# Kernel tuning notes

Hardware: AMD Instinct MI355X
Metric: run time of the kernel (lower is better)

## Reference

```python
import jax, jax.numpy as jnp
import numpy as np

B, D, N = 32768, 128, 8
TEMP = 0.25          # episodic_memory_temperature
DECAY = 0.99         # episodic_strength_decay
AGE_INC = 0.02       # episodic_age_increment


def _l2norm(x, eps=1e-6):
    n = jnp.sqrt(jnp.sum(x * x, axis=-1, keepdims=True))
    return x / jnp.maximum(n, eps)


def setup_inputs() -> dict:
    key = jax.random.key(0)
    ks = jax.random.split(key, 16)
    s = 0.05
    inp = {
        'signal': jax.random.normal(ks[0], (B, D), jnp.float32),
        'previous': jax.random.normal(ks[1], (B, D), jnp.float32),
        'hidden': jax.random.normal(ks[2], (B, D), jnp.float32),
        'episodic_keys': jax.random.normal(ks[3], (B, N, D), jnp.float32),
        'episodic_values': jax.random.normal(ks[4], (B, N, D), jnp.float32),
        'episodic_strength': jax.random.uniform(ks[5], (B, N), jnp.float32),
        'episodic_age': jax.random.uniform(ks[6], (B, N), jnp.float32),
        # Linear weights stored as [in, out] (torch stores [out, in]); small random
        # instead of the zero init so gradients flow for kernel testing.
        'w_read_query': jax.random.normal(ks[7], (2 * D, D), jnp.float32) * s,
        'w_read_mix': jax.random.normal(ks[8], (2 * D, 1), jnp.float32) * s,
        'b_read_mix': jnp.full((1,), -0.2, jnp.float32),
        'w_key': jax.random.normal(ks[9], (2 * D, D), jnp.float32) * s,
        'b_key': jnp.zeros((D,), jnp.float32),
        'w_value': jax.random.normal(ks[10], (2 * D, D), jnp.float32) * s,
        'b_value': jnp.zeros((D,), jnp.float32),
        'w_write': jax.random.normal(ks[11], (2 * D, 1), jnp.float32) * s,
        'b_write': jnp.full((1,), -0.6, jnp.float32),
        'w_persist': jax.random.normal(ks[12], (2 * D, 1), jnp.float32) * s,
        'b_persist': jnp.zeros((1,), jnp.float32),
        'w_merge': jax.random.normal(ks[13], (2 * D, 1), jnp.float32) * s,
        'b_merge': jnp.zeros((1,), jnp.float32),
    }
    return inp


def reference(signal, previous, hidden, episodic_keys, episodic_values,
              episodic_strength, episodic_age,
              w_read_query, w_read_mix, b_read_mix, w_key, b_key, w_value,
              b_value, w_write, b_write, w_persist, b_persist, w_merge, b_merge):
    dtype = signal.dtype
    n_slots = episodic_keys.shape[1]

    # ---------------- read ----------------
    sp = jnp.concatenate([signal, previous], axis=-1)             # [B, 2D]
    query = _l2norm(sp @ w_read_query)                            # [B, D]
    norm_keys = _l2norm(episodic_keys)                            # [B, N, D]
    content_scores = jnp.einsum('bd,bnd->bn', query, norm_keys)   # [B, N]
    content_w = jax.nn.softmax(content_scores / TEMP, axis=-1)
    content_read = jnp.einsum('bn,bnd->bd', content_w, episodic_values)
    persistent_scores = 2.4 * episodic_strength + 0.6 * (1.0 - episodic_age)
    persistent_w = jax.nn.softmax(persistent_scores / TEMP, axis=-1)
    persistent_read = jnp.einsum('bn,bnd->bd', persistent_w, episodic_values)
    read_mix = jax.nn.sigmoid(sp @ w_read_mix + b_read_mix)       # [B, 1]
    memory_read = read_mix * content_read + (1.0 - read_mix) * persistent_read

    # ---------------- write ----------------
    joined = jnp.concatenate([signal, hidden], axis=-1)           # [B, 2D]
    candidate_key = jnp.tanh(joined @ w_key + b_key)              # [B, D]
    candidate_value = jnp.tanh(joined @ w_value + b_value)        # [B, D]
    write_strength = jax.nn.sigmoid(joined @ w_write + b_write)   # [B, 1]
    persistence = jax.nn.sigmoid(joined @ w_persist + b_persist)  # [B, 1]
    similarity = jnp.einsum('bd,bnd->bn', _l2norm(candidate_key), norm_keys)

    top_k = min(3, n_slots)
    top_sim, top_idx = jax.lax.top_k(similarity, top_k)           # [B, 3]
    max_sim = top_sim[:, 0]
    merge_index = top_idx[:, 0]
    second_sim = top_sim[:, 1]
    novelty = jnp.clip(1.0 - max_sim, 0.0, 1.0)[:, None]          # [B, 1]

    replace_scores = (1.2 * episodic_age + 1.0 * (1.0 - episodic_strength)
                      + 0.5 * (1.0 - similarity))
    replace_index = jnp.argmax(replace_scores, axis=-1)
    merge_pref = jax.nn.sigmoid(joined @ w_merge + b_merge + 2.6 * max_sim[:, None])

    full_m = (max_sim > 0.78) & (merge_pref[:, 0] >= 0.55)
    multi_m = full_m & (second_sim > 0.68)
    partial_m = (~multi_m) & (max_sim > 0.64) & (second_sim > 0.52)

    rows = jnp.arange(signal.shape[0])[:, None]
    target_w = jax.nn.one_hot(replace_index, n_slots, dtype=dtype)
    partial_w = jax.nn.softmax(top_sim[:, :2] / TEMP, axis=-1)
    partial_target = jnp.zeros_like(target_w).at[rows, top_idx[:, :2]].add(partial_w)
    multi_w = jax.nn.softmax(top_sim / TEMP, axis=-1)
    multi_target = jnp.zeros_like(target_w).at[rows, top_idx].add(multi_w)
    full_target = jax.nn.one_hot(merge_index, n_slots, dtype=dtype)

    target_w = jnp.where(full_m[:, None], full_target, target_w)
    target_w = jnp.where(partial_m[:, None], partial_target, target_w)
    target_w = jnp.where(multi_m[:, None], multi_target, target_w)

    scale = jnp.where(multi_m[:, None], 0.16 + 0.52 * write_strength,
                      jnp.where(partial_m[:, None], 0.18 + 0.62 * write_strength,
                                0.20 + 0.80 * write_strength))
    overwrite = target_w * scale * (0.55 + 0.45 * novelty)        # [B, N]
    ow3 = overwrite[..., None]                                    # [B, N, 1]

    merge_like = full_m | partial_m | multi_m
    key_mix = jnp.where(merge_like[:, None], 0.28 + 0.24 * persistence,
                        0.78 + 0.16 * persistence)[:, :, None]    # [B, 1, 1]
    value_mix = jnp.where(merge_like[:, None], 0.42 + 0.28 * persistence,
                          0.82 + 0.12 * persistence)[:, :, None]

    updated_keys = episodic_keys + ow3 * key_mix * (candidate_key[:, None, :] - episodic_keys)
    updated_values = episodic_values + ow3 * value_mix * (candidate_value[:, None, :] - episodic_values)

    boost = overwrite * (0.45 + 0.35 * persistence + 0.45 * novelty + 0.25 * write_strength)
    updated_strength = jnp.clip(episodic_strength * DECAY + boost, 0.0, 1.0)
    updated_age = jnp.clip((episodic_age + AGE_INC) * (1.0 - overwrite), 0.0, 1.0)

    return memory_read, updated_keys, updated_values, updated_strength, updated_age
```

## Files before the change

### kernel.cpp

```cpp
#include <hip/hip_runtime.h>
#include <cstddef>

#define BD 128
#define NS 8
#define ROWS 32
#define BLOCK 256

typedef float __attribute__((ext_vector_type(2))) f32x2;

__device__ __forceinline__ float sigm(float x) { return 1.0f / (1.0f + __expf(-x)); }

__device__ __forceinline__ void nt_store2(float2 v, float2* p) {
    f32x2 t; t.x = v.x; t.y = v.y;
    __builtin_nontemporal_store(t, (f32x2*)p);
}

__global__ __launch_bounds__(BLOCK, 3)
void sbcore_kernel(
    const float* __restrict__ g_signal, const float* __restrict__ g_prev,
    const float* __restrict__ g_hidden, const float* __restrict__ g_keys,
    const float* __restrict__ g_vals, const float* __restrict__ g_str,
    const float* __restrict__ g_age,
    const float* __restrict__ w_rq, const float* __restrict__ w_mix,
    const float* __restrict__ b_mix, const float* __restrict__ w_key,
    const float* __restrict__ b_key, const float* __restrict__ w_val,
    const float* __restrict__ b_val, const float* __restrict__ w_wr,
    const float* __restrict__ b_wr, const float* __restrict__ w_pe,
    const float* __restrict__ b_pe, const float* __restrict__ w_mg,
    const float* __restrict__ b_mg,
    float* __restrict__ o_read, float* __restrict__ o_keys,
    float* __restrict__ o_vals, float* __restrict__ o_str,
    float* __restrict__ o_age)
{
    __shared__ __align__(16) float sig_s[ROWS][BD];
    __shared__ __align__(16) float prv_s[ROWS][BD];
    __shared__ __align__(16) float hid_s[ROWS][BD];
    __shared__ __align__(16) float str_s[ROWS*NS], age_s[ROWS*NS];
    __shared__ float red_s[4][16][2];
    __shared__ float ckinv_s[ROWS];
    __shared__ __align__(16) float head_s[ROWS][4];

    const int tid = threadIdx.x;
    const int row0 = blockIdx.x * ROWS;

    {
        const float4* gs4 = (const float4*)(g_signal + (size_t)row0 * BD);
        const float4* gp4 = (const float4*)(g_prev   + (size_t)row0 * BD);
        const float4* gh4 = (const float4*)(g_hidden + (size_t)row0 * BD);
#pragma unroll
        for (int it = 0; it < (ROWS*BD/4)/BLOCK; ++it) {
            int i = tid + it*BLOCK;
            int r = i >> 5, d4 = i & 31;
            *(float4*)&sig_s[r][d4*4] = gs4[i];
            *(float4*)&prv_s[r][d4*4] = gp4[i];
            *(float4*)&hid_s[r][d4*4] = gh4[i];
        }
    }
    str_s[tid] = g_str[(size_t)row0*NS + tid];
    age_s[tid] = g_age[(size_t)row0*NS + tid];
    __syncthreads();

    {
        const int hr = tid >> 3;
        const int hh = (tid >> 1) & 3;
        const int hj = tid & 1;
        const float* ws = (hh==0) ? w_mix : (hh==1) ? w_wr : (hh==2) ? w_pe : w_mg;
        const float4* w4p = (const float4*)(ws + hj*BD);
        const float*  xr  = (hj==0) ? &sig_s[hr][0]
                                    : ((hh==0) ? &prv_s[hr][0] : &hid_s[hr][0]);
        const float4* x4p = (const float4*)xr;
        float p = 0.f;
#pragma unroll
        for (int q = 0; q < 32; ++q) {
            const float4 w4 = w4p[q];
            const float4 x4 = x4p[q];
            p = fmaf(x4.w, w4.w, fmaf(x4.z, w4.z, fmaf(x4.y, w4.y, fmaf(x4.x, w4.x, p))));
        }
        p += __shfl_xor(p, 1);
        if (hj == 0) head_s[hr][hh] = p;
    }

    const int d    = tid & (BD-1);
    const int h    = tid >> 7;
    const int wave = tid >> 6;
    const int lane = tid & 63;

    float aq[16], ak[16], av[16];
#pragma unroll
    for (int r = 0; r < 16; ++r) { aq[r] = 0.f; ak[r] = 0.f; av[r] = 0.f; }

    for (int kk = 0; kk < BD; kk += 4) {
        float wq0 = w_rq[(kk+0)*BD + d], wq1 = w_rq[(kk+1)*BD + d],
              wq2 = w_rq[(kk+2)*BD + d], wq3 = w_rq[(kk+3)*BD + d];
        float wk0 = w_key[(kk+0)*BD + d], wk1 = w_key[(kk+1)*BD + d],
              wk2 = w_key[(kk+2)*BD + d], wk3 = w_key[(kk+3)*BD + d];
        float wv0 = w_val[(kk+0)*BD + d], wv1 = w_val[(kk+1)*BD + d],
              wv2 = w_val[(kk+2)*BD + d], wv3 = w_val[(kk+3)*BD + d];
#pragma unroll
        for (int r = 0; r < 16; ++r) {
            const float4 s4 = *(const float4*)&sig_s[h*16 + r][kk];
            aq[r] = fmaf(s4.w, wq3, fmaf(s4.z, wq2, fmaf(s4.y, wq1, fmaf(s4.x, wq0, aq[r]))));
            ak[r] = fmaf(s4.w, wk3, fmaf(s4.z, wk2, fmaf(s4.y, wk1, fmaf(s4.x, wk0, ak[r]))));
            av[r] = fmaf(s4.w, wv3, fmaf(s4.z, wv2, fmaf(s4.y, wv1, fmaf(s4.x, wv0, av[r]))));
        }
    }
    for (int kk = 0; kk < BD; kk += 4) {
        const int k = kk + BD;
        float wq0 = w_rq[(k+0)*BD + d], wq1 = w_rq[(k+1)*BD + d],
              wq2 = w_rq[(k+2)*BD + d], wq3 = w_rq[(k+3)*BD + d];
        float wk0 = w_key[(k+0)*BD + d], wk1 = w_key[(k+1)*BD + d],
              wk2 = w_key[(k+2)*BD + d], wk3 = w_key[(k+3)*BD + d];
        float wv0 = w_val[(k+0)*BD + d], wv1 = w_val[(k+1)*BD + d],
              wv2 = w_val[(k+2)*BD + d], wv3 = w_val[(k+3)*BD + d];
#pragma unroll
        for (int r = 0; r < 16; ++r) {
            const float4 p4 = *(const float4*)&prv_s[h*16 + r][kk];
            const float4 h4 = *(const float4*)&hid_s[h*16 + r][kk];
            aq[r] = fmaf(p4.w, wq3, fmaf(p4.z, wq2, fmaf(p4.y, wq1, fmaf(p4.x, wq0, aq[r]))));
            ak[r] = fmaf(h4.w, wk3, fmaf(h4.z, wk2, fmaf(h4.y, wk1, fmaf(h4.x, wk0, ak[r]))));
            av[r] = fmaf(h4.w, wv3, fmaf(h4.z, wv2, fmaf(h4.y, wv1, fmaf(h4.x, wv0, av[r]))));
        }
    }

    const float bk = b_key[d], bv = b_val[d];
    float ckr[16], cvr[16], q2[16], c2[16];
#pragma unroll
    for (int r = 0; r < 16; ++r) {
        ckr[r] = tanhf(ak[r] + bk);
        cvr[r] = tanhf(av[r] + bv);
        q2[r]  = aq[r] * aq[r];
        c2[r]  = ckr[r] * ckr[r];
    }
#pragma unroll
    for (int off = 32; off > 0; off >>= 1) {
#pragma unroll
        for (int r = 0; r < 16; ++r) {
            q2[r] += __shfl_xor(q2[r], off);
            c2[r] += __shfl_xor(c2[r], off);
        }
    }
    if (lane == 0) {
#pragma unroll
        for (int r = 0; r < 16; ++r) { red_s[wave][r][0] = q2[r]; red_s[wave][r][1] = c2[r]; }
    }
    __syncthreads();
#pragma unroll
    for (int r = 0; r < 16; ++r) {
        float sq = red_s[h*2][r][0] + red_s[h*2+1][r][0];
        float sc = red_s[h*2][r][1] + red_s[h*2+1][r][1];
        float qi = 1.0f / fmaxf(sqrtf(sq), 1e-6f);
        sig_s[h*16 + r][d] = aq[r] * qi;
        prv_s[h*16 + r][d] = ckr[r];
        hid_s[h*16 + r][d] = cvr[r];
        if (d == 0) ckinv_s[h*16 + r] = 1.0f / fmaxf(sqrtf(sc), 1e-6f);
    }
    __syncthreads();

    const float bmix = b_mix[0], bwr = b_wr[0], bpe = b_pe[0], bmg = b_mg[0];
    const int sj = lane & 7;

    for (int rr = 0; rr < 8; ++rr) {
        const int r = wave*8 + rr;
        const size_t row = (size_t)row0 + r;
        const size_t kvb = row * (size_t)(NS*BD);

        const float4* kp4  = (const float4*)(g_keys + kvb);
        const float4* qrow = (const float4*)&sig_s[r][0];
        const float4* crow = (const float4*)&prv_s[r][0];
        float pk = 0.f, pq = 0.f, pc = 0.f;
#pragma unroll
        for (int q = 0; q < 4; ++q) {
            const float4 k4 = kp4[4*lane + q];
            const float4 q4 = qrow[sj*4 + q];
            const float4 c4 = crow[sj*4 + q];
            pk = fmaf(k4.w,k4.w, fmaf(k4.z,k4.z, fmaf(k4.y,k4.y, fmaf(k4.x,k4.x, pk))));
            pq = fmaf(q4.w,k4.w, fmaf(q4.z,k4.z, fmaf(q4.y,k4.y, fmaf(q4.x,k4.x, pq))));
            pc = fmaf(c4.w,k4.w, fmaf(c4.z,k4.z, fmaf(c4.y,k4.y, fmaf(c4.x,k4.x, pc))));
        }
        const float2* vp = (const float2*)(g_vals + kvb);
        float2 vf[NS];
#pragma unroll
        for (int n = 0; n < NS; ++n) vf[n] = vp[n*64 + lane];
        const float2 cki = *(const float2*)&prv_s[r][2*lane];
        const float2 cvi = *(const float2*)&hid_s[r][2*lane];

        pk += __shfl_xor(pk, 1); pk += __shfl_xor(pk, 2); pk += __shfl_xor(pk, 4);
        pq += __shfl_xor(pq, 1); pq += __shfl_xor(pq, 2); pq += __shfl_xor(pq, 4);
        pc += __shfl_xor(pc, 1); pc += __shfl_xor(pc, 2); pc += __shfl_xor(pc, 4);
        const float ki   = 1.0f / fmaxf(sqrtf(pk), 1e-6f);
        const float csn  = pq * ki;
        const float simn = pc * ki * ckinv_s[r];
        float cs[NS], sim[NS];
#pragma unroll
        for (int m = 0; m < NS; ++m) {
            cs[m]  = __shfl(csn,  m*8);
            sim[m] = __shfl(simn, m*8);
        }

        const float4 hd = *(const float4*)&head_s[r][0];
        const float mix   = sigm(hd.x + bmix);
        const float wsv   = sigm(hd.y + bwr);
        const float pev   = sigm(hd.z + bpe);
        const float mglin = hd.w + bmg;

        float mC = cs[0];
#pragma unroll
        for (int n = 1; n < NS; ++n) mC = fmaxf(mC, cs[n]);
        float eC[NS], sC = 0.f;
#pragma unroll
        for (int n = 0; n < NS; ++n) { eC[n] = __expf((cs[n]-mC)*4.0f); sC += eC[n]; }
        const float4 st0 = *(const float4*)&str_s[r*NS];
        const float4 st1 = *(const float4*)&str_s[r*NS+4];
        const float4 ag0 = *(const float4*)&age_s[r*NS];
        const float4 ag1 = *(const float4*)&age_s[r*NS+4];
        const float stv[NS] = {st0.x,st0.y,st0.z,st0.w,st1.x,st1.y,st1.z,st1.w};
        const float agv[NS] = {ag0.x,ag0.y,ag0.z,ag0.w,ag1.x,ag1.y,ag1.z,ag1.w};
        float psc[NS]; float mP = -1e30f;
#pragma unroll
        for (int n = 0; n < NS; ++n) {
            psc[n] = fmaf(2.4f, stv[n], 0.6f*(1.0f - agv[n]));
            mP = fmaxf(mP, psc[n]);
        }
        float eP[NS], sP = 0.f;
#pragma unroll
        for (int n = 0; n < NS; ++n) { eP[n] = __expf((psc[n]-mP)*4.0f); sP += eP[n]; }
        const float icS = 1.0f/sC, ipS = 1.0f/sP;

        float2 cr = make_float2(0.f, 0.f), prd = make_float2(0.f, 0.f);
#pragma unroll
        for (int n = 0; n < NS; ++n) {
            float wc = eC[n]*icS, wp = eP[n]*ipS;
            cr.x  = fmaf(wc, vf[n].x, cr.x);  cr.y  = fmaf(wc, vf[n].y, cr.y);
            prd.x = fmaf(wp, vf[n].x, prd.x); prd.y = fmaf(wp, vf[n].y, prd.y);
        }
        float2 mr;
        mr.x = mix*cr.x + (1.0f-mix)*prd.x;
        mr.y = mix*cr.y + (1.0f-mix)*prd.y;
        nt_store2(mr, &((float2*)(o_read + row*BD))[lane]);

        float tv0 = -1e30f; int ti0 = 0;
#pragma unroll
        for (int n = 0; n < NS; ++n) if (sim[n] > tv0) { tv0 = sim[n]; ti0 = n; }
        float tv1 = -1e30f; int ti1 = 0;
#pragma unroll
        for (int n = 0; n < NS; ++n) {
            float v = (n == ti0) ? -1e30f : sim[n];
            if (v > tv1) { tv1 = v; ti1 = n; }
        }
        float tv2 = -1e30f; int ti2 = 0;
#pragma unroll
        for (int n = 0; n < NS; ++n) {
            float v = (n == ti0 || n == ti1) ? -1e30f : sim[n];
            if (v > tv2) { tv2 = v; ti2 = n; }
        }

        float rm = -1e30f; int ri = 0;
#pragma unroll
        for (int n = 0; n < NS; ++n) {
            float rsv = fmaf(1.2f, agv[n], (1.0f - stv[n])) + 0.5f*(1.0f - sim[n]);
            if (rsv > rm) { rm = rsv; ri = n; }
        }

        const float mpref = sigm(mglin + 2.6f*tv0);
        const bool full  = (tv0 > 0.78f) && (mpref >= 0.55f);
        const bool multi = full && (tv1 > 0.68f);
        const bool part  = (!multi) && (tv0 > 0.64f) && (tv1 > 0.52f);
        const float nov  = fminf(fmaxf(1.0f - tv0, 0.0f), 1.0f);

        float a0, a1, a2, aR;
        if (multi) {
            float e1 = __expf((tv1 - tv0)*4.0f), e2 = __expf((tv2 - tv0)*4.0f);
            float inv = 1.0f/(1.0f + e1 + e2);
            a0 = inv; a1 = e1*inv; a2 = e2*inv; aR = 0.f;
        } else if (part) {
            float e1 = __expf((tv1 - tv0)*4.0f);
            float inv = 1.0f/(1.0f + e1);
            a0 = inv; a1 = e1*inv; a2 = 0.f; aR = 0.f;
        } else if (full) {
            a0 = 1.f; a1 = 0.f; a2 = 0.f; aR = 0.f;
        } else {
            a0 = 0.f; a1 = 0.f; a2 = 0.f; aR = 1.f;
        }

        const float scl = multi ? fmaf(0.52f, wsv, 0.16f)
                        : part  ? fmaf(0.62f, wsv, 0.18f)
                                : fmaf(0.80f, wsv, 0.20f);
        const bool  mlike = full || part || multi;
        const float km  = mlike ? fmaf(0.24f, pev, 0.28f) : fmaf(0.16f, pev, 0.78f);
        const float vm  = mlike ? fmaf(0.28f, pev, 0.42f) : fmaf(0.12f, pev, 0.82f);
        const float owc = scl * fmaf(0.45f, nov, 0.55f);
        const float bco = 0.45f + 0.35f*pev + 0.45f*nov + 0.25f*wsv;

        const float2* kp2 = (const float2*)(g_keys + kvb);
        float2* okp = (float2*)(o_keys + kvb);
        float2* ovp = (float2*)(o_vals + kvb);
#pragma unroll
        for (int n = 0; n < NS; ++n) {
            const float2 kf2 = kp2[n*64 + lane];
            float tn = ((n==ti0) ? a0 : (n==ti1) ? a1 : (n==ti2) ? a2 : 0.f)
                     + ((n==ri) ? aR : 0.f);
            float ow = tn*owc;
            float a = ow*km, b2 = ow*vm;
            float2 uk, uv;
            uk.x = fmaf(a,  cki.x - kf2.x, kf2.x);
            uk.y = fmaf(a,  cki.y - kf2.y, kf2.y);
            uv.x = fmaf(b2, cvi.x - vf[n].x, vf[n].x);
            uv.y = fmaf(b2, cvi.y - vf[n].y, vf[n].y);
            nt_store2(uk, &okp[n*64 + lane]);
            nt_store2(uv, &ovp[n*64 + lane]);
        }
        if (lane < NS) {
            float tn = ((lane==ti0) ? a0 : (lane==ti1) ? a1 : (lane==ti2) ? a2 : 0.f)
                     + ((lane==ri) ? aR : 0.f);
            float ow = tn*owc;
            float us = fminf(fmaxf(fmaf(str_s[r*NS+lane], 0.99f, ow*bco), 0.f), 1.f);
            float ua = fminf(fmaxf((age_s[r*NS+lane] + 0.02f)*(1.0f - ow), 0.f), 1.f);
            o_str[row*NS + lane] = us;
            o_age[row*NS + lane] = ua;
        }
    }
}

extern "C" void kernel_launch(void* const* d_in, const int* in_sizes, int n_in,
                              void* d_out, int out_size, void* d_ws, size_t ws_size,
                              hipStream_t stream) {
    const float* g_signal = (const float*)d_in[0];
    const float* g_prev   = (const float*)d_in[1];
    const float* g_hidden = (const float*)d_in[2];
    const float* g_keys   = (const float*)d_in[3];
    const float* g_vals   = (const float*)d_in[4];
    const float* g_str    = (const float*)d_in[5];
    const float* g_age    = (const float*)d_in[6];
    const float* w_rq     = (const float*)d_in[7];
    const float* w_mix    = (const float*)d_in[8];
    const float* b_mix    = (const float*)d_in[9];
    const float* w_key    = (const float*)d_in[10];
    const float* b_key    = (const float*)d_in[11];
    const float* w_val    = (const float*)d_in[12];
    const float* b_val    = (const float*)d_in[13];
    const float* w_wr     = (const float*)d_in[14];
    const float* b_wr     = (const float*)d_in[15];
    const float* w_pe     = (const float*)d_in[16];
    const float* b_pe     = (const float*)d_in[17];
    const float* w_mg     = (const float*)d_in[18];
    const float* b_mg     = (const float*)d_in[19];

    const size_t B = (size_t)in_sizes[0] / BD;
    float* out   = (float*)d_out;
    float* o_read = out;
    float* o_keys = o_read + B*BD;
    float* o_vals = o_keys + B*NS*BD;
    float* o_str  = o_vals + B*NS*BD;
    float* o_age  = o_str  + B*NS;

    const int blocks = (int)(B / ROWS);
    sbcore_kernel<<<dim3(blocks), dim3(BLOCK), 0, stream>>>(
        g_signal, g_prev, g_hidden, g_keys, g_vals, g_str, g_age,
        w_rq, w_mix, b_mix, w_key, b_key, w_val, b_val,
        w_wr, b_wr, w_pe, b_pe, w_mg, b_mg,
        o_read, o_keys, o_vals, o_str, o_age);
}
```

Measured before the change: 651.1 us.

## Shrink block to 4 rows and split projection K across waves

Cuts rows per block from 32 to 4, so the grid grows eightfold and each wave handles one memory row. The three projection matmuls are reorganised so each wave covers a K-slice with float4 weight columns, and partial sums are reduced through shared memory. The 4 per-row head dot products are now spread over 16 lanes each. This aims for more parallelism and latency hiding in the memory-bound phase, at the cost of rereading the three weight matrices far more often (eight times as many blocks) and adding an extra reduction step.

Measured after the change: 613.3 us. 1.06x faster.

```diff
diff --git a/kernel.cpp b/kernel.cpp
--- a/kernel.cpp
+++ b/kernel.cpp
@@ -3,9 +3,10 @@
 
 #define BD 128
 #define NS 8
-#define ROWS 32
+#define ROWS 4
 #define BLOCK 256
 
+typedef float __attribute__((ext_vector_type(4))) f32x4;
 typedef float __attribute__((ext_vector_type(2))) f32x2;
 
 __device__ __forceinline__ float sigm(float x) { return 1.0f / (1.0f + __expf(-x)); }
@@ -35,132 +36,153 @@
     __shared__ __align__(16) float sig_s[ROWS][BD];
     __shared__ __align__(16) float prv_s[ROWS][BD];
     __shared__ __align__(16) float hid_s[ROWS][BD];
-    __shared__ __align__(16) float str_s[ROWS*NS], age_s[ROWS*NS];
-    __shared__ float red_s[4][16][2];
-    __shared__ float ckinv_s[ROWS];
+    __shared__ __align__(16) f32x4 part_s[4][3][ROWS][32];
+    __shared__ float str_s[ROWS*NS], age_s[ROWS*NS];
     __shared__ __align__(16) float head_s[ROWS][4];
 
     const int tid = threadIdx.x;
     const int row0 = blockIdx.x * ROWS;
 
+    if (tid < ROWS*32) {
+        int r = tid >> 5, d4 = tid & 31;
+        size_t gb = (size_t)(row0 + r) * 32 + d4;
+        *(float4*)&sig_s[r][d4*4] = ((const float4*)g_signal)[gb];
+        *(float4*)&prv_s[r][d4*4] = ((const float4*)g_prev)[gb];
+        *(float4*)&hid_s[r][d4*4] = ((const float4*)g_hidden)[gb];
+    }
+    if (tid < ROWS*NS) {
+        str_s[tid] = g_str[(size_t)row0*NS + tid];
+        age_s[tid] = g_age[(size_t)row0*NS + tid];
+    }
+    __syncthreads();
+
     {
-        const float4* gs4 = (const float4*)(g_signal + (size_t)row0 * BD);
-        const float4* gp4 = (const float4*)(g_prev   + (size_t)row0 * BD);
-        const float4* gh4 = (const float4*)(g_hidden + (size_t)row0 * BD);
-#pragma unroll
-        for (int it = 0; it < (ROWS*BD/4)/BLOCK; ++it) {
-            int i = tid + it*BLOCK;
-            int r = i >> 5, d4 = i & 31;
-            *(float4*)&sig_s[r][d4*4] = gs4[i];
-            *(float4*)&prv_s[r][d4*4] = gp4[i];
-            *(float4*)&hid_s[r][d4*4] = gh4[i];
-        }
-    }
-    str_s[tid] = g_str[(size_t)row0*NS + tid];
-    age_s[tid] = g_age[(size_t)row0*NS + tid];
-    __syncthreads();
-
-    {
-        const int hr = tid >> 3;
-        const int hh = (tid >> 1) & 3;
-        const int hj = tid & 1;
+        const int dotid = tid >> 4;
+        const int hr = dotid >> 2;
+        const int hh = dotid & 3;
+        const int hj = tid & 15;
         const float* ws = (hh==0) ? w_mix : (hh==1) ? w_wr : (hh==2) ? w_pe : w_mg;
-        const float4* w4p = (const float4*)(ws + hj*BD);
-        const float*  xr  = (hj==0) ? &sig_s[hr][0]
-                                    : ((hh==0) ? &prv_s[hr][0] : &hid_s[hr][0]);
-        const float4* x4p = (const float4*)xr;
+        const float* xb = (hj < 8) ? &sig_s[hr][0]
+                        : (((hh==0) ? &prv_s[hr][0] : &hid_s[hr][0]) - BD);
         float p = 0.f;
 #pragma unroll
-        for (int q = 0; q < 32; ++q) {
-            const float4 w4 = w4p[q];
-            const float4 x4 = x4p[q];
+        for (int q = 0; q < 4; ++q) {
+            const int k = hj*16 + q*4;
+            const float4 w4 = *(const float4*)&ws[k];
+            const float4 x4 = *(const float4*)&xb[k];
             p = fmaf(x4.w, w4.w, fmaf(x4.z, w4.z, fmaf(x4.y, w4.y, fmaf(x4.x, w4.x, p))));
         }
-        p += __shfl_xor(p, 1);
+        p += __shfl_xor(p, 1); p += __shfl_xor(p, 2);
+        p += __shfl_xor(p, 4); p += __shfl_xor(p, 8);
         if (hj == 0) head_s[hr][hh] = p;
     }
 
-    const int d    = tid & (BD-1);
-    const int h    = tid >> 7;
     const int wave = tid >> 6;
     const int lane = tid & 63;
-
-    float aq[16], ak[16], av[16];
-#pragma unroll
-    for (int r = 0; r < 16; ++r) { aq[r] = 0.f; ak[r] = 0.f; av[r] = 0.f; }
-
-    for (int kk = 0; kk < BD; kk += 4) {
-        float wq0 = w_rq[(kk+0)*BD + d], wq1 = w_rq[(kk+1)*BD + d],
-              wq2 = w_rq[(kk+2)*BD + d], wq3 = w_rq[(kk+3)*BD + d];
-        float wk0 = w_key[(kk+0)*BD + d], wk1 = w_key[(kk+1)*BD + d],
-              wk2 = w_key[(kk+2)*BD + d], wk3 = w_key[(kk+3)*BD + d];
-        float wv0 = w_val[(kk+0)*BD + d], wv1 = w_val[(kk+1)*BD + d],
-              wv2 = w_val[(kk+2)*BD + d], wv3 = w_val[(kk+3)*BD + d];
-#pragma unroll
-        for (int r = 0; r < 16; ++r) {
-            const float4 s4 = *(const float4*)&sig_s[h*16 + r][kk];
-            aq[r] = fmaf(s4.w, wq3, fmaf(s4.z, wq2, fmaf(s4.y, wq1, fmaf(s4.x, wq0, aq[r]))));
-            ak[r] = fmaf(s4.w, wk3, fmaf(s4.z, wk2, fmaf(s4.y, wk1, fmaf(s4.x, wk0, ak[r]))));
-            av[r] = fmaf(s4.w, wv3, fmaf(s4.z, wv2, fmaf(s4.y, wv1, fmaf(s4.x, wv0, av[r]))));
-        }
-    }
-    for (int kk = 0; kk < BD; kk += 4) {
-        const int k = kk + BD;
-        float wq0 = w_rq[(k+0)*BD + d], wq1 = w_rq[(k+1)*BD + d],
-              wq2 = w_rq[(k+2)*BD + d], wq3 = w_rq[(k+3)*BD + d];
-        float wk0 = w_key[(k+0)*BD + d], wk1 = w_key[(k+1)*BD + d],
-              wk2 = w_key[(k+2)*BD + d], wk3 = w_key[(k+3)*BD + d];
-        float wv0 = w_val[(k+0)*BD + d], wv1 = w_val[(k+1)*BD + d],
-              wv2 = w_val[(k+2)*BD + d], wv3 = w_val[(k+3)*BD + d];
-#pragma unroll
-        for (int r = 0; r < 16; ++r) {
-            const float4 p4 = *(const float4*)&prv_s[h*16 + r][kk];
-            const float4 h4 = *(const float4*)&hid_s[h*16 + r][kk];
-            aq[r] = fmaf(p4.w, wq3, fmaf(p4.z, wq2, fmaf(p4.y, wq1, fmaf(p4.x, wq0, aq[r]))));
-            ak[r] = fmaf(h4.w, wk3, fmaf(h4.z, wk2, fmaf(h4.y, wk1, fmaf(h4.x, wk0, ak[r]))));
-            av[r] = fmaf(h4.w, wv3, fmaf(h4.z, wv2, fmaf(h4.y, wv1, fmaf(h4.x, wv0, av[r]))));
-        }
-    }
-
-    const float bk = b_key[d], bv = b_val[d];
-    float ckr[16], cvr[16], q2[16], c2[16];
-#pragma unroll
-    for (int r = 0; r < 16; ++r) {
-        ckr[r] = tanhf(ak[r] + bk);
-        cvr[r] = tanhf(av[r] + bv);
-        q2[r]  = aq[r] * aq[r];
-        c2[r]  = ckr[r] * ckr[r];
-    }
-#pragma unroll
-    for (int off = 32; off > 0; off >>= 1) {
-#pragma unroll
-        for (int r = 0; r < 16; ++r) {
-            q2[r] += __shfl_xor(q2[r], off);
-            c2[r] += __shfl_xor(c2[r], off);
-        }
-    }
-    if (lane == 0) {
-#pragma unroll
-        for (int r = 0; r < 16; ++r) { red_s[wave][r][0] = q2[r]; red_s[wave][r][1] = c2[r]; }
+    const int hi   = lane >> 5;
+    const int dg   = lane & 31;
+
+    {
+        const int kbase = hi ? (BD + wave*32) : (wave*32);
+        const f32x4* wq4 = (const f32x4*)w_rq;
+        const f32x4* wk4 = (const f32x4*)w_key;
+        const f32x4* wv4 = (const f32x4*)w_val;
+        const int wi0 = kbase*32 + dg;
+        const float* x1b = hi ? &prv_s[0][0] : &sig_s[0][0];
+        const float* x2b = hi ? &hid_s[0][0] : &sig_s[0][0];
+        const int xo = wave*32;
+
+        f32x4 aq[ROWS], ak[ROWS], av[ROWS];
+#pragma unroll
+        for (int r = 0; r < ROWS; ++r) { aq[r] = 0.f; ak[r] = 0.f; av[r] = 0.f; }
+
+#pragma unroll 2
+        for (int j = 0; j < 8; ++j) {
+            const int kj = j*4;
+            f32x4 w0 = wq4[wi0 + (kj+0)*32], w1 = wq4[wi0 + (kj+1)*32],
+                  w2 = wq4[wi0 + (kj+2)*32], w3 = wq4[wi0 + (kj+3)*32];
+#pragma unroll
+            for (int r = 0; r < ROWS; ++r) {
+                const f32x4 x1 = *(const f32x4*)&x1b[r*BD + xo + kj];
+                aq[r] += x1.x*w0; aq[r] += x1.y*w1; aq[r] += x1.z*w2; aq[r] += x1.w*w3;
+            }
+            f32x4 k0 = wk4[wi0 + (kj+0)*32], k1 = wk4[wi0 + (kj+1)*32],
+                  k2 = wk4[wi0 + (kj+2)*32], k3 = wk4[wi0 + (kj+3)*32];
+            f32x4 v0 = wv4[wi0 + (kj+0)*32], v1 = wv4[wi0 + (kj+1)*32],
+                  v2 = wv4[wi0 + (kj+2)*32], v3 = wv4[wi0 + (kj+3)*32];
+#pragma unroll
+            for (int r = 0; r < ROWS; ++r) {
+                const f32x4 x2 = *(const f32x4*)&x2b[r*BD + xo + kj];
+                ak[r] += x2.x*k0; ak[r] += x2.y*k1; ak[r] += x2.z*k2; ak[r] += x2.w*k3;
+                av[r] += x2.x*v0; av[r] += x2.y*v1; av[r] += x2.z*v2; av[r] += x2.w*v3;
+            }
+        }
+
+#pragma unroll
+        for (int r = 0; r < ROWS; ++r) {
+            f32x4 t;
+            t.x = __shfl_xor(aq[r].x, 32); t.y = __shfl_xor(aq[r].y, 32);
+            t.z = __shfl_xor(aq[r].z, 32); t.w = __shfl_xor(aq[r].w, 32);
+            aq[r] += t;
+            t.x = __shfl_xor(ak[r].x, 32); t.y = __shfl_xor(ak[r].y, 32);
+            t.z = __shfl_xor(ak[r].z, 32); t.w = __shfl_xor(ak[r].w, 32);
+            ak[r] += t;
+            t.x = __shfl_xor(av[r].x, 32); t.y = __shfl_xor(av[r].y, 32);
+            t.z = __shfl_xor(av[r].z, 32); t.w = __shfl_xor(av[r].w, 32);
+            av[r] += t;
+        }
+        if (!hi) {
+#pragma unroll
+            for (int r = 0; r < ROWS; ++r) {
+                part_s[wave][0][r][dg] = aq[r];
+                part_s[wave][1][r][dg] = ak[r];
+                part_s[wave][2][r][dg] = av[r];
+            }
+        }
     }
     __syncthreads();
-#pragma unroll
-    for (int r = 0; r < 16; ++r) {
-        float sq = red_s[h*2][r][0] + red_s[h*2+1][r][0];
-        float sc = red_s[h*2][r][1] + red_s[h*2+1][r][1];
-        float qi = 1.0f / fmaxf(sqrtf(sq), 1e-6f);
-        sig_s[h*16 + r][d] = aq[r] * qi;
-        prv_s[h*16 + r][d] = ckr[r];
-        hid_s[h*16 + r][d] = cvr[r];
-        if (d == 0) ckinv_s[h*16 + r] = 1.0f / fmaxf(sqrtf(sc), 1e-6f);
+
+    const int r = wave;
+    float ckinv_reg;
+    {
+        const int dgf = lane >> 1;
+        const int co  = (lane & 1) * 2;
+        float2 sq = make_float2(0.f, 0.f), sk = make_float2(0.f, 0.f),
+               sv = make_float2(0.f, 0.f);
+#pragma unroll
+        for (int pw = 0; pw < 4; ++pw) {
+            const float* pq = (const float*)&part_s[pw][0][r][dgf];
+            const float* pk = (const float*)&part_s[pw][1][r][dgf];
+            const float* pv = (const float*)&part_s[pw][2][r][dgf];
+            const float2 tq = *(const float2*)&pq[co];
+            const float2 tk = *(const float2*)&pk[co];
+            const float2 tv = *(const float2*)&pv[co];
+            sq.x += tq.x; sq.y += tq.y;
+            sk.x += tk.x; sk.y += tk.y;
+            sv.x += tv.x; sv.y += tv.y;
+        }
+        const float2 bk2 = *(const float2*)&b_key[2*lane];
+        const float2 bv2 = *(const float2*)&b_val[2*lane];
+        const float ckx = tanhf(sk.x + bk2.x), cky = tanhf(sk.y + bk2.y);
+        const float cvx = tanhf(sv.x + bv2.x), cvy = tanhf(sv.y + bv2.y);
+        float q2 = sq.x*sq.x + sq.y*sq.y;
+        float c2 = ckx*ckx + cky*cky;
+#pragma unroll
+        for (int off = 32; off > 0; off >>= 1) {
+            q2 += __shfl_xor(q2, off);
+            c2 += __shfl_xor(c2, off);
+        }
+        const float qinv = 1.0f / fmaxf(sqrtf(q2), 1e-6f);
+        ckinv_reg = 1.0f / fmaxf(sqrtf(c2), 1e-6f);
+        *(float2*)&sig_s[r][2*lane] = make_float2(sq.x*qinv, sq.y*qinv);
+        *(float2*)&prv_s[r][2*lane] = make_float2(ckx, cky);
+        *(float2*)&hid_s[r][2*lane] = make_float2(cvx, cvy);
     }
     __syncthreads();
 
     const float bmix = b_mix[0], bwr = b_wr[0], bpe = b_pe[0], bmg = b_mg[0];
     const int sj = lane & 7;
-
-    for (int rr = 0; rr < 8; ++rr) {
-        const int r = wave*8 + rr;
+    {
         const size_t row = (size_t)row0 + r;
         const size_t kvb = row * (size_t)(NS*BD);
 
@@ -189,7 +211,7 @@
         pc += __shfl_xor(pc, 1); pc += __shfl_xor(pc, 2); pc += __shfl_xor(pc, 4);
         const float ki   = 1.0f / fmaxf(sqrtf(pk), 1e-6f);
         const float csn  = pq * ki;
-        const float simn = pc * ki * ckinv_s[r];
+        const float simn = pc * ki * ckinv_reg;
         float cs[NS], sim[NS];
 #pragma unroll
         for (int m = 0; m < NS; ++m) {
```
